# Optimization experiments

Measured on AMD Instinct MI355X. Metric: run time of the kernel, lower is better.

Reference implementation:

```python
import math
import jax, jax.numpy as jnp
import numpy as np

S, B, H = 2048, 1, 4096
NH, HD = 32, 128          # heads, head dim
ROT = HD // 2             # rotary dim per 2D-RoPE half = 64


def rotate_half(x):
    x1, x2 = jnp.split(x, 2, axis=-1)
    return jnp.concatenate([-x2, x1], axis=-1)


def rope_tables(seq_len, dim, base=10000.0):
    inv_freq = 1.0 / (base ** (jnp.arange(0, dim, 2, dtype=jnp.float32) / dim))
    freqs = jnp.arange(seq_len, dtype=jnp.float32)[:, None] * inv_freq[None, :]
    emb = jnp.concatenate([freqs, freqs], axis=-1)  # [S, dim]
    return jnp.cos(emb), jnp.sin(emb)


def apply_rope(q, k, cos, sin, pos):
    # q,k: [S,B,NH,ROT]; pos: [S,B] -> gather cos/sin per token
    c = cos[pos][:, :, None, :]  # [S,B,1,ROT]
    s = sin[pos][:, :, None, :]
    return q * c + rotate_half(q) * s, k * c + rotate_half(k) * s


def setup_inputs() -> dict:
    key = jax.random.key(0)
    ks = jax.random.split(key, 5)
    hidden_states = jax.random.normal(ks[0], (S, B, H), dtype=jnp.float32)
    pos = jnp.arange(S, dtype=jnp.int64 if jax.config.jax_enable_x64 else jnp.int32)
    position_ids = jnp.stack([pos, pos])[None]  # [B=1, 2, S]
    attention_mask = jnp.triu(jnp.ones((S, S), dtype=bool), k=1)[None, None]  # True = masked
    scale = 0.02
    wqkv = jax.random.normal(ks[1], (3 * H, H), dtype=jnp.float32) * scale
    bqkv = jax.random.normal(ks[2], (3 * H,), dtype=jnp.float32) * scale
    wdense = jax.random.normal(ks[3], (H, H), dtype=jnp.float32) * scale
    bdense = jax.random.normal(ks[4], (H,), dtype=jnp.float32) * scale
    return {"hidden_states": hidden_states, "position_ids": position_ids,
            "attention_mask": attention_mask, "wqkv": wqkv, "bqkv": bqkv,
            "wdense": wdense, "bdense": bdense, "layer_id": 1}


def reference(hidden_states, position_ids, attention_mask, wqkv, bqkv, wdense, bdense, layer_id):
    s, b, h = hidden_states.shape
    # fused QKV projection: [S,B,NH,3*HD]
    mixed = (jnp.einsum('sbh,oh->sbo', hidden_states, wqkv) + bqkv).reshape(s, b, NH, 3 * HD)
    q, k, v = jnp.split(mixed, 3, axis=-1)  # each [S,B,NH,HD]

    # 2D RoPE: split head dim in half, rotate each half with its own position ids
    q1, q2 = jnp.split(q, 2, axis=-1)
    k1, k2 = jnp.split(k, 2, axis=-1)
    cos, sin = rope_tables(s, ROT)
    pos = position_ids[:, 0, :].T       # [S,B]
    block_pos = position_ids[:, 1, :].T  # [S,B]
    q1, k1 = apply_rope(q1, k1, cos, sin, pos)
    q2, k2 = apply_rope(q2, k2, cos, sin, block_pos)
    q = jnp.concatenate([q1, q2], axis=-1)
    k = jnp.concatenate([k1, k2], axis=-1)

    # layer-scaled attention (ChatGLM style)
    coeff = float(layer_id + 1)
    q = q / (math.sqrt(HD) * coeff)
    scores = jnp.einsum('sbhd,tbhd->bhst', q, k)  # [B,NH,S,S]
    scores = jnp.where(attention_mask, jnp.float32(-10000.0), scores)
    scores = scores.astype(jnp.float32) * coeff
    probs = jax.nn.softmax(scores, axis=-1).astype(q.dtype)
    context = jnp.einsum('bhst,tbhd->sbhd', probs, v).reshape(s, b, h)

    out = jnp.einsum('sbh,oh->sbo', context, wdense) + bdense
    return out
```

## Files before the change

kernel.cpp:

```cpp
#include <hip/hip_runtime.h>

typedef unsigned short u16;
typedef unsigned int u32;
typedef __attribute__((ext_vector_type(4))) float f32x4;
typedef __attribute__((ext_vector_type(16))) float f32x16;
typedef __attribute__((ext_vector_type(8))) short bf16x8;
typedef __attribute__((ext_vector_type(2))) unsigned int u32x2;

#define S_LEN 2048
#define NHEAD 32
#define HDD 128
#define HID 4096
#define N_QKV 12288
#define KDIM 4096
#define RS 12288

__device__ __forceinline__ u16 f2bf(float f) {
  u32 u = __builtin_bit_cast(u32, f);
  u = (u + 0x7FFFu + ((u >> 16) & 1u)) >> 16;
  return (u16)u;
}
__device__ __forceinline__ float bf2f(u16 h) {
  u32 u = ((u32)h) << 16;
  return __builtin_bit_cast(float, u);
}

__device__ __forceinline__ int gkey(int line) { return (line ^ (line >> 1)) & 7; }

__device__ __forceinline__ void gl2lds16(const void* g, void* l) {
  __builtin_amdgcn_global_load_lds(
      (const __attribute__((address_space(1))) u32*)g,
      (__attribute__((address_space(3))) u32*)l, 16, 0, 0);
}

#define FULL_BAR()                          \
  {                                         \
    asm volatile("" ::: "memory");          \
    __builtin_amdgcn_s_barrier();           \
    asm volatile("" ::: "memory");          \
  }

__global__ __launch_bounds__(256) void cvt3_kernel(const float* __restrict__ s0, u16* __restrict__ d0, int n0,
                                                   const float* __restrict__ s2, u16* __restrict__ d2, int n2,
                                                   float* __restrict__ cos_t, float* __restrict__ sin_t) {
  int i = blockIdx.x * blockDim.x + threadIdx.x;
  if (i < S_LEN * 32) {
    int s = i >> 5, ii = i & 31;
    float invf = expf(-0.28782313662425572f * (float)ii);
    float a = (float)s * invf;
    cos_t[i] = cosf(a);
    sin_t[i] = sinf(a);
  }
  int st = gridDim.x * blockDim.x;
  int ntot = n0 + n2;
  for (; i < ntot; i += st) {
    const float* s;
    u16* d;
    int j = i;
    if (j < n0) {
      s = s0; d = d0;
    } else {
      j -= n0; s = s2; d = d2;
    }
    float4 v = ((const float4*)s)[j];
    u32x2 o;
    o.x = (u32)f2bf(v.x) | ((u32)f2bf(v.y) << 16);
    o.y = (u32)f2bf(v.z) | ((u32)f2bf(v.w) << 16);
    ((u32x2*)d)[j] = o;
  }
}

__global__ __launch_bounds__(256) void ropek_kernel(u16* __restrict__ mixed,
                                                    const int* __restrict__ pid,
                                                    const float* __restrict__ cos_t,
                                                    const float* __restrict__ sin_t) {
  int idx = blockIdx.x * blockDim.x + threadIdx.x;
  const int total = NHEAD * S_LEN * 2 * 8;
  if (idx >= total) return;
  int j = idx & 7;
  int half = (idx >> 3) & 1;
  int s = (idx >> 4) & (S_LEN - 1);
  int h = idx >> 15;
  int i0 = j * 4;
  int p = pid[half * S_LEN + s];
  float4 c4 = *(const float4*)(cos_t + p * 32 + i0);
  float4 s4 = *(const float4*)(sin_t + p * 32 + i0);
  u16* base = mixed + (size_t)s * RS + h * 384 + 128 + half * 64 + i0;
  ushort4 x1v = *(const ushort4*)(base);
  ushort4 x2v = *(const ushort4*)(base + 32);
  ushort4 o1, o2;
  {
    float x1 = bf2f(x1v.x), x2 = bf2f(x2v.x);
    o1.x = f2bf(x1 * c4.x - x2 * s4.x);
    o2.x = f2bf(x2 * c4.x + x1 * s4.x);
  }
  {
    float x1 = bf2f(x1v.y), x2 = bf2f(x2v.y);
    o1.y = f2bf(x1 * c4.y - x2 * s4.y);
    o2.y = f2bf(x2 * c4.y + x1 * s4.y);
  }
  {
    float x1 = bf2f(x1v.z), x2 = bf2f(x2v.z);
    o1.z = f2bf(x1 * c4.z - x2 * s4.z);
    o2.z = f2bf(x2 * c4.z + x1 * s4.z);
  }
  {
    float x1 = bf2f(x1v.w), x2 = bf2f(x2v.w);
    o1.w = f2bf(x1 * c4.w - x2 * s4.w);
    o2.w = f2bf(x2 * c4.w + x1 * s4.w);
  }
  *(ushort4*)(base) = o1;
  *(ushort4*)(base + 32) = o2;
}

__global__ __launch_bounds__(512, 2) void gemmQ(const u16* __restrict__ A,
                                                const u16* __restrict__ B,
                                                const float* __restrict__ bias,
                                                u16* __restrict__ outb) {
  __shared__ __align__(16) char lds[3][40960];

  const int tid = threadIdx.x;
  const int lane = tid & 63, w = tid >> 6;
  const int l31 = lane & 31, hh = lane >> 5;
  const int wm = w >> 2, wn = w & 3;

  int x = blockIdx.x & 7, loc = blockIdx.x >> 3;
  int mb = loc & 7, nb = x * 4 + (loc >> 3);
  const int bm = mb * 256, bn = nb * 384;

  f32x16 acc[4][3];
#pragma unroll
  for (int mi = 0; mi < 4; ++mi)
#pragma unroll
    for (int ni = 0; ni < 3; ++ni)
#pragma unroll
      for (int r = 0; r < 16; ++r) acc[mi][ni][r] = 0.f;

  const size_t K2 = (size_t)KDIM * 2;

  const char* gA[2];
#pragma unroll
  for (int j = 0; j < 2; ++j) {
    int slot = j * 512 + tid;
    int line = slot >> 3;
    int sl = (slot & 7) ^ gkey(line);
    int row = 2 * line + (sl >> 2);
    int colb = (sl & 3) * 16;
    gA[j] = (const char*)A + (size_t)(bm + row) * K2 + colb;
  }
  const char* gB[3];
#pragma unroll
  for (int j = 0; j < 3; ++j) {
    int slot = j * 512 + tid;
    int line = slot >> 3;
    int sl = (slot & 7) ^ gkey(line);
    int row = 2 * line + (sl >> 2);
    int colb = (sl & 3) * 16;
    gB[j] = (const char*)B + (size_t)(bn + row) * K2 + colb;
  }
  const int ldst = w * 1024;

#define QIA(t, bi)                                                  \
  {                                                                 \
    char* Lb = lds[bi];                                             \
    gl2lds16(gA[0] + (size_t)(t) * 64, Lb + ldst);                  \
    gl2lds16(gA[1] + (size_t)(t) * 64, Lb + 8192 + ldst);           \
  }
#define QIB(t, bi)                                                  \
  {                                                                 \
    char* Lb = lds[bi] + 16384;                                     \
    _Pragma("unroll")                                               \
    for (int j = 0; j < 3; ++j)                                     \
      gl2lds16(gB[j] + (size_t)(t) * 64, Lb + j * 8192 + ldst);     \
  }

  int offA[4][2], offB[3][2];
#pragma unroll
  for (int mi = 0; mi < 4; ++mi) {
    int r = wm * 128 + mi * 32 + l31;
    int line = r >> 1;
#pragma unroll
    for (int kk = 0; kk < 2; ++kk) {
      int sl = (((r & 1) << 2) + kk * 2 + hh) ^ gkey(line);
      offA[mi][kk] = line * 128 + sl * 16;
    }
  }
#pragma unroll
  for (int ni = 0; ni < 3; ++ni) {
    int r = wn * 96 + ni * 32 + l31;
    int line = r >> 1;
#pragma unroll
    for (int kk = 0; kk < 2; ++kk) {
      int sl = (((r & 1) << 2) + kk * 2 + hh) ^ gkey(line);
      offB[ni][kk] = 16384 + line * 128 + sl * 16;
    }
  }

  QIA(0, 0); QIB(0, 0);
  QIA(1, 1); QIB(1, 1);
  asm volatile("s_waitcnt vmcnt(5)" ::: "memory");
  FULL_BAR();

  int cur = 0, nx2 = 2;
  for (int kt = 0; kt < 128; ++kt) {
    const char* buf = lds[cur];
    const bool pf = (kt + 2) < 128;
    bf16x8 a[4], b[3];
#pragma unroll
    for (int mi = 0; mi < 4; ++mi) a[mi] = *(const bf16x8*)(buf + offA[mi][0]);
#pragma unroll
    for (int ni = 0; ni < 3; ++ni) b[ni] = *(const bf16x8*)(buf + offB[ni][0]);
    if (pf) QIA(kt + 2, nx2);
    FULL_BAR();
    __builtin_amdgcn_s_setprio(1);
#pragma unroll
    for (int mi = 0; mi < 4; ++mi)
#pragma unroll
      for (int ni = 0; ni < 3; ++ni)
        acc[mi][ni] = __builtin_amdgcn_mfma_f32_32x32x16_bf16(a[mi], b[ni], acc[mi][ni], 0, 0, 0);
    __builtin_amdgcn_s_setprio(0);
#pragma unroll
    for (int mi = 0; mi < 4; ++mi) a[mi] = *(const bf16x8*)(buf + offA[mi][1]);
#pragma unroll
    for (int ni = 0; ni < 3; ++ni) b[ni] = *(const bf16x8*)(buf + offB[ni][1]);
    if (pf) {
      QIB(kt + 2, nx2);
      asm volatile("s_waitcnt vmcnt(5)" ::: "memory");
    } else if (kt == 126) {
      asm volatile("s_waitcnt vmcnt(0)" ::: "memory");
    }
    FULL_BAR();
    __builtin_amdgcn_s_setprio(1);
#pragma unroll
    for (int mi = 0; mi < 4; ++mi)
#pragma unroll
      for (int ni = 0; ni < 3; ++ni)
        acc[mi][ni] = __builtin_amdgcn_mfma_f32_32x32x16_bf16(a[mi], b[ni], acc[mi][ni], 0, 0, 0);
    __builtin_amdgcn_s_setprio(0);
    cur = (cur + 1 == 3) ? 0 : cur + 1;
    nx2 = (nx2 + 1 == 3) ? 0 : nx2 + 1;
  }
#undef QIA
#undef QIB

#pragma unroll
  for (int ni = 0; ni < 3; ++ni) {
    int n = bn + wn * 96 + ni * 32 + l31;
    float bv = bias[n];
#pragma unroll
    for (int mi = 0; mi < 4; ++mi) {
      int m0 = bm + wm * 128 + mi * 32 + 4 * hh;
#pragma unroll
      for (int reg = 0; reg < 16; ++reg) {
        int row = m0 + (reg & 3) + 8 * (reg >> 2);
        outb[(size_t)row * N_QKV + n] = f2bf(acc[mi][ni][reg] + bv);
      }
    }
  }
}

__global__ __launch_bounds__(512, 2) void gemmD(const u16* __restrict__ A,
                                                const float* __restrict__ Bf,
                                                const float* __restrict__ bias,
                                                float* __restrict__ outf) {
  __shared__ __align__(16) char lds[2][49152];

  const int tid = threadIdx.x;
  const int lane = tid & 63, w = tid >> 6;
  const int l31 = lane & 31, hh = lane >> 5;
  const int wm = w >> 1, wn = w & 1;

  int x = blockIdx.x & 7, loc = blockIdx.x >> 3;
  int mb = loc & 7, nb = x * 4 + (loc >> 3);
  const int bm = mb * 256, bn = nb * 128;

  f32x16 acc[2][2];
#pragma unroll
  for (int mi = 0; mi < 2; ++mi)
#pragma unroll
    for (int ni = 0; ni < 2; ++ni)
#pragma unroll
      for (int r = 0; r < 16; ++r) acc[mi][ni][r] = 0.f;

  const size_t K2 = (size_t)KDIM * 2;

  const char* gA[2];
#pragma unroll
  for (int j = 0; j < 2; ++j) {
    int slot = j * 512 + tid;
    int line = slot >> 3;
    int sl = (slot & 7) ^ gkey(line);
    int row = 2 * line + (sl >> 2);
    int colb = (sl & 3) * 16;
    gA[j] = (const char*)A + (size_t)(bm + row) * K2 + colb;
  }
  int bline = tid >> 3;
  int bsl = tid & 7;
  int brow = 2 * bline + (bsl >> 2);
  int bcole = (bsl & 3) * 8;
  const float* gBs = Bf + (size_t)(bn + brow) * KDIM + bcole;
  int bphys = bsl ^ gkey(bline);
  const int bwr = 32768 + bline * 128 + bphys * 16;
  const int ldst = w * 1024;

#define DIA(t, kk)                                                            \
  {                                                                           \
    char* Lb = lds[(t) & 1] + (kk) * 16384;                                   \
    gl2lds16(gA[0] + (size_t)(t) * 128 + (kk) * 64, Lb + ldst);               \
    gl2lds16(gA[1] + (size_t)(t) * 128 + (kk) * 64, Lb + 8192 + ldst);        \
  }
#define DGB(t)                                                                \
  {                                                                           \
    const float* p0 = gBs + (size_t)(t) * 64;                                 \
    b0a = *(const float4*)(p0);                                               \
    b0b = *(const float4*)(p0 + 4);                                           \
    b1a = *(const float4*)(p0 + 32);                                          \
    b1b = *(const float4*)(p0 + 36);                                          \
  }
#define DWB(t)                                                                \
  {                                                                           \
    bf16x8 o0, o1;                                                            \
    o0[0] = (short)f2bf(b0a.x); o0[1] = (short)f2bf(b0a.y);                   \
    o0[2] = (short)f2bf(b0a.z); o0[3] = (short)f2bf(b0a.w);                   \
    o0[4] = (short)f2bf(b0b.x); o0[5] = (short)f2bf(b0b.y);                   \
    o0[6] = (short)f2bf(b0b.z); o0[7] = (short)f2bf(b0b.w);                   \
    o1[0] = (short)f2bf(b1a.x); o1[1] = (short)f2bf(b1a.y);                   \
    o1[2] = (short)f2bf(b1a.z); o1[3] = (short)f2bf(b1a.w);                   \
    o1[4] = (short)f2bf(b1b.x); o1[5] = (short)f2bf(b1b.y);                   \
    o1[6] = (short)f2bf(b1b.z); o1[7] = (short)f2bf(b1b.w);                   \
    char* Lb = lds[(t) & 1];                                                  \
    *(bf16x8*)(Lb + bwr) = o0;                                                \
    *(bf16x8*)(Lb + 8192 + bwr) = o1;                                         \
  }

  int offA[2][2][2], offB[2][2][2];
#pragma unroll
  for (int mi = 0; mi < 2; ++mi) {
    int r = wm * 64 + mi * 32 + l31;
    int line = r >> 1;
#pragma unroll
    for (int kku = 0; kku < 2; ++kku)
#pragma unroll
      for (int st = 0; st < 2; ++st) {
        int sl = (((r & 1) << 2) + st * 2 + hh) ^ gkey(line);
        offA[mi][kku][st] = kku * 16384 + line * 128 + sl * 16;
      }
  }
#pragma unroll
  for (int ni = 0; ni < 2; ++ni) {
    int r = wn * 64 + ni * 32 + l31;
    int line = r >> 1;
#pragma unroll
    for (int kku = 0; kku < 2; ++kku)
#pragma unroll
      for (int st = 0; st < 2; ++st) {
        int sl = (((r & 1) << 2) + st * 2 + hh) ^ gkey(line);
        offB[ni][kku][st] = 32768 + kku * 8192 + line * 128 + sl * 16;
      }
  }

  float4 b0a, b0b, b1a, b1b;
  DGB(0);
  DIA(0, 0);
  DIA(0, 1);
  asm volatile("s_waitcnt vmcnt(4)" ::: "memory");
  DWB(0);
  asm volatile("s_waitcnt vmcnt(0) lgkmcnt(0)" ::: "memory");
  FULL_BAR();

  for (int kt = 0; kt < 64; ++kt) {
    const char* buf = lds[kt & 1];
    const bool pf = (kt + 1) < 64;
    bf16x8 a[2][2], b[2][2];
#pragma unroll
    for (int mi = 0; mi < 2; ++mi)
#pragma unroll
      for (int st = 0; st < 2; ++st) a[mi][st] = *(const bf16x8*)(buf + offA[mi][0][st]);
#pragma unroll
    for (int ni = 0; ni < 2; ++ni)
#pragma unroll
      for (int st = 0; st < 2; ++st) b[ni][st] = *(const bf16x8*)(buf + offB[ni][0][st]);
    if (pf) {
      DIA(kt + 1, 0);
      DGB(kt + 1);
      asm volatile("s_waitcnt vmcnt(6)" ::: "memory");
    } else {
      asm volatile("s_waitcnt vmcnt(0)" ::: "memory");
    }
    FULL_BAR();
    __builtin_amdgcn_s_setprio(1);
#pragma unroll
    for (int st = 0; st < 2; ++st)
#pragma unroll
      for (int mi = 0; mi < 2; ++mi)
#pragma unroll
        for (int ni = 0; ni < 2; ++ni)
          acc[mi][ni] = __builtin_amdgcn_mfma_f32_32x32x16_bf16(a[mi][st], b[ni][st], acc[mi][ni], 0, 0, 0);
    __builtin_amdgcn_s_setprio(0);
#pragma unroll
    for (int mi = 0; mi < 2; ++mi)
#pragma unroll
      for (int st = 0; st < 2; ++st) a[mi][st] = *(const bf16x8*)(buf + offA[mi][1][st]);
#pragma unroll
    for (int ni = 0; ni < 2; ++ni)
#pragma unroll
      for (int st = 0; st < 2; ++st) b[ni][st] = *(const bf16x8*)(buf + offB[ni][1][st]);
    if (pf) {
      DIA(kt + 1, 1);
      asm volatile("s_waitcnt vmcnt(2)" ::: "memory");
      DWB(kt + 1);
      asm volatile("s_waitcnt lgkmcnt(0)" ::: "memory");
    }
    FULL_BAR();
    __builtin_amdgcn_s_setprio(1);
#pragma unroll
    for (int st = 0; st < 2; ++st)
#pragma unroll
      for (int mi = 0; mi < 2; ++mi)
#pragma unroll
        for (int ni = 0; ni < 2; ++ni)
          acc[mi][ni] = __builtin_amdgcn_mfma_f32_32x32x16_bf16(a[mi][st], b[ni][st], acc[mi][ni], 0, 0, 0);
    __builtin_amdgcn_s_setprio(0);
  }
#undef DIA
#undef DGB
#undef DWB

#pragma unroll
  for (int ni = 0; ni < 2; ++ni) {
    int n = bn + wn * 64 + ni * 32 + l31;
    float bv = bias[n];
#pragma unroll
    for (int mi = 0; mi < 2; ++mi) {
      int m0 = bm + wm * 64 + mi * 32 + 4 * hh;
#pragma unroll
      for (int reg = 0; reg < 16; ++reg) {
        int row = m0 + (reg & 3) + 8 * (reg >> 2);
        outf[(size_t)row * HID + n] = acc[mi][ni][reg] + bv;
      }
    }
  }
}

__global__ __launch_bounds__(512) void attn_kernel(const u16* __restrict__ mixed,
                                                   const int* __restrict__ pid,
                                                   const float* __restrict__ cos_t,
                                                   const float* __restrict__ sin_t,
                                                   u16* __restrict__ ctx) {
  __shared__ __align__(16) u16 Ksh[2][64 * 136];
  __shared__ __align__(16) u16 Vsh[2][128 * 64];
  __shared__ __align__(16) u16 Pt[8][16 * 72];

  int tid = threadIdx.x;
  int lane = tid & 63, w = tid >> 6;
  int lane15 = lane & 15, g = lane >> 4;

  int bpg = blockIdx.x & 7;
  int h = blockIdx.x >> 3;

  const u16* qp = mixed + (size_t)h * 384;
  const u16* kp = mixed + (size_t)h * 384 + 128;
  const u16* vp = mixed + (size_t)h * 384 + 256;

  int krow = tid >> 3, kc = (tid & 7) * 16;
  int vk0 = 2 * (tid & 31), vd0 = (tid >> 5) * 8;
  f32x4 z4 = {0.f, 0.f, 0.f, 0.f};
  const float QSC = 0.08838834764831845f;
  const float L2E = 1.4426950408889634f;

  bf16x8 kx0, kx1, vr0, vr1;
#define ALOAD(t)                                                              \
  {                                                                           \
    const u16* kr = kp + (size_t)((t)*64 + krow) * RS + kc;                   \
    kx0 = *(const bf16x8*)kr;                                                 \
    kx1 = *(const bf16x8*)(kr + 8);                                           \
    const u16* vr = vp + (size_t)((t)*64 + vk0) * RS + vd0;                   \
    vr0 = *(const bf16x8*)vr;                                                 \
    vr1 = *(const bf16x8*)(vr + RS);                                          \
  }
#define AWRITE(bb)                                                            \
  {                                                                           \
    *(bf16x8*)(&Ksh[bb][krow * 136 + kc]) = kx0;                              \
    *(bf16x8*)(&Ksh[bb][krow * 136 + kc + 8]) = kx1;                          \
    _Pragma("unroll") for (int jj = 0; jj < 8; ++jj) {                        \
      int d = vd0 + jj;                                                       \
      u32 val = (u32)(u16)vr0[jj] | ((u32)(u16)vr1[jj] << 16);                \
      *(u32*)((char*)Vsh[bb] + d * 128 + (((vk0 >> 3) ^ (d & 7)) << 4) +      \
              (vk0 & 7) * 2) = val;                                           \
    }                                                                         \
  }

  for (int pass = 0; pass < 2; ++pass) {
    int pg = pass ? (15 - bpg) : bpg;
    int qi = 2 * pg + (w >> 2);
    int qrow = qi * 64 + (w & 3) * 16 + lane15;
    int ntiles = 2 * pg + 2;

    bf16x8 qf[4];
    const u16* qptr = qp + (size_t)qrow * RS + g * 8;
#pragma unroll
    for (int d0 = 0; d0 < 4; ++d0) qf[d0] = *(const bf16x8*)(qptr + d0 * 32);
    {
      int p1 = pid[qrow], p2 = pid[S_LEN + qrow];
      float cc[8], ss[8], dd[8], tt[8];
#pragma unroll
      for (int j = 0; j < 8; ++j) {
        cc[j] = cos_t[p1 * 32 + g * 8 + j];
        ss[j] = sin_t[p1 * 32 + g * 8 + j];
        dd[j] = cos_t[p2 * 32 + g * 8 + j];
        tt[j] = sin_t[p2 * 32 + g * 8 + j];
      }
#pragma unroll
      for (int j = 0; j < 8; ++j) {
        float x1 = bf2f((u16)qf[0][j]), x2 = bf2f((u16)qf[1][j]);
        qf[0][j] = (short)f2bf((x1 * cc[j] - x2 * ss[j]) * QSC);
        qf[1][j] = (short)f2bf((x2 * cc[j] + x1 * ss[j]) * QSC);
        float y1 = bf2f((u16)qf[2][j]), y2 = bf2f((u16)qf[3][j]);
        qf[2][j] = (short)f2bf((y1 * dd[j] - y2 * tt[j]) * QSC);
        qf[3][j] = (short)f2bf((y2 * dd[j] + y1 * tt[j]) * QSC);
      }
    }

    f32x4 pv[8];
#pragma unroll
    for (int db = 0; db < 8; ++db) pv[db] = z4;
    float m_run = -1e30f, l_run = 0.0f;

    ALOAD(0);
    AWRITE(0);
    __syncthreads();

    for (int t = 0; t < ntiles; ++t) {
      const u16* Kc = Ksh[t & 1];
      const char* Vc = (const char*)Vsh[t & 1];
      if (t + 1 < ntiles) ALOAD(t + 1);

      int kb0 = t * 64;
      f32x4 sa[4];
#pragma unroll
      for (int kt16 = 0; kt16 < 4; ++kt16) sa[kt16] = z4;
#pragma unroll
      for (int kt16 = 0; kt16 < 4; ++kt16)
#pragma unroll
        for (int d0 = 0; d0 < 4; ++d0) {
          bf16x8 kf = *(const bf16x8*)(Kc + (kt16 * 16 + lane15) * 136 + d0 * 32 + g * 8);
          sa[kt16] = __builtin_amdgcn_mfma_f32_16x16x32_bf16(kf, qf[d0], sa[kt16], 0, 0, 0);
        }
      float s[16];
#pragma unroll
      for (int kt16 = 0; kt16 < 4; ++kt16)
#pragma unroll
        for (int rr = 0; rr < 4; ++rr) {
          int kg = kb0 + kt16 * 16 + 4 * g + rr;
          s[kt16 * 4 + rr] = (kg > qrow) ? -1e30f : sa[kt16][rr];
        }
      float mx = s[0];
#pragma unroll
      for (int i2 = 1; i2 < 16; ++i2) mx = fmaxf(mx, s[i2]);
      mx = fmaxf(mx, __shfl_xor(mx, 16));
      mx = fmaxf(mx, __shfl_xor(mx, 32));
      if (!__all(mx - m_run <= 8.0f)) {
        float mnew = fmaxf(m_run, mx);
        float fac = exp2f((m_run - mnew) * L2E);
        l_run *= fac;
#pragma unroll
        for (int db = 0; db < 8; ++db) pv[db] *= fac;
        m_run = mnew;
      }
      float p[16], psum = 0.f;
#pragma unroll
      for (int i2 = 0; i2 < 16; ++i2) {
        p[i2] = exp2f((s[i2] - m_run) * L2E);
        psum += p[i2];
      }
      psum += __shfl_xor(psum, 16);
      psum += __shfl_xor(psum, 32);
      l_run += psum;

#pragma unroll
      for (int kt16 = 0; kt16 < 4; ++kt16) {
        u32x2 pw;
        pw.x = (u32)f2bf(p[kt16 * 4 + 0]) | ((u32)f2bf(p[kt16 * 4 + 1]) << 16);
        pw.y = (u32)f2bf(p[kt16 * 4 + 2]) | ((u32)f2bf(p[kt16 * 4 + 3]) << 16);
        *(u32x2*)(&Pt[w][lane15 * 72 + kt16 * 16 + 4 * g]) = pw;
      }
      asm volatile("s_waitcnt lgkmcnt(0)" ::: "memory");
      bf16x8 pf0 = *(const bf16x8*)(&Pt[w][lane15 * 72 + 8 * g]);
      bf16x8 pf1 = *(const bf16x8*)(&Pt[w][lane15 * 72 + 32 + 8 * g]);

#pragma unroll
      for (int db = 0; db < 8; ++db) {
        int d = db * 16 + lane15;
        bf16x8 vf0 = *(const bf16x8*)(Vc + d * 128 + ((g ^ (d & 7)) << 4));
        bf16x8 vf1 = *(const bf16x8*)(Vc + d * 128 + (((4 + g) ^ (d & 7)) << 4));
        pv[db] = __builtin_amdgcn_mfma_f32_16x16x32_bf16(vf0, pf0, pv[db], 0, 0, 0);
        pv[db] = __builtin_amdgcn_mfma_f32_16x16x32_bf16(vf1, pf1, pv[db], 0, 0, 0);
      }

      if (t + 1 < ntiles) AWRITE((t + 1) & 1);
      __syncthreads();
    }

    float inv = 1.0f / l_run;
#pragma unroll
    for (int db = 0; db < 8; ++db) {
      ushort4 o;
      o.x = f2bf(pv[db][0] * inv);
      o.y = f2bf(pv[db][1] * inv);
      o.z = f2bf(pv[db][2] * inv);
      o.w = f2bf(pv[db][3] * inv);
      *(ushort4*)(ctx + (size_t)qrow * HID + h * HDD + db * 16 + 4 * g) = o;
    }
    __syncthreads();
  }
#undef ALOAD
#undef AWRITE
}

extern "C" void kernel_launch(void* const* d_in, const int* in_sizes, int n_in,
                              void* d_out, int out_size, void* d_ws, size_t ws_size,
                              hipStream_t stream) {
  const float* hidden = (const float*)d_in[0];
  const int* pid = (const int*)d_in[1];
  const float* wqkv = (const float*)d_in[3];
  const float* bqkv = (const float*)d_in[4];
  const float* wdense = (const float*)d_in[5];
  const float* bdense = (const float*)d_in[6];
  float* out = (float*)d_out;

  char* ws = (char*)d_ws;
  u16* W1 = (u16*)ws;
  u16* X = (u16*)(ws + 134217728);
  u16* mixed = (u16*)(ws + 150994944);
  u16* ctx = (u16*)(ws + 201326592);
  float* cos_t = (float*)(ws + 218103808);
  float* sin_t = (float*)(ws + 218365952);

  cvt3_kernel<<<dim3(2048), dim3(256), 0, stream>>>(
      wqkv, W1, N_QKV * KDIM / 4, hidden, X, S_LEN * HID / 4, cos_t, sin_t);

  gemmQ<<<dim3(256), dim3(512), 0, stream>>>(X, W1, bqkv, mixed);

  ropek_kernel<<<dim3(4096), dim3(256), 0, stream>>>(mixed, pid, cos_t, sin_t);

  attn_kernel<<<dim3(256), dim3(512), 0, stream>>>(mixed, pid, cos_t, sin_t, ctx);

  gemmD<<<dim3(256), dim3(512), 0, stream>>>(ctx, wdense, bdense, out);
}
```

Measured before the change: 453.9 us.

## Split attention into one 64-row query tile per block, heaviest tiles first

Attention work is reorganized from 256 blocks of 512 threads, each running two balanced passes over paired causal query groups, into 1024 blocks of 256 threads. Each block handles a single 64-row query tile, and blocks are ordered so the longest causal tiles launch first. K/V staging is widened so each thread loads more data per tile. The log2(e) factor is also folded into the Q scale, which removes multiplies from the softmax exponent path. The change gives the scheduler more blocks to balance and likely higher occupancy, at the cost of each K/V tile being reloaded by more blocks.

```diff
diff --git a/kernel.cpp b/kernel.cpp
--- a/kernel.cpp
+++ b/kernel.cpp
@@ -442,176 +442,174 @@
   }
 }
 
-__global__ __launch_bounds__(512) void attn_kernel(const u16* __restrict__ mixed,
+__global__ __launch_bounds__(256) void attn_kernel(const u16* __restrict__ mixed,
                                                    const int* __restrict__ pid,
                                                    const float* __restrict__ cos_t,
                                                    const float* __restrict__ sin_t,
                                                    u16* __restrict__ ctx) {
   __shared__ __align__(16) u16 Ksh[2][64 * 136];
   __shared__ __align__(16) u16 Vsh[2][128 * 64];
-  __shared__ __align__(16) u16 Pt[8][16 * 72];
+  __shared__ __align__(16) u16 Pt[4][16 * 72];
 
   int tid = threadIdx.x;
   int lane = tid & 63, w = tid >> 6;
   int lane15 = lane & 15, g = lane >> 4;
 
-  int bpg = blockIdx.x & 7;
-  int h = blockIdx.x >> 3;
+  int qslot = blockIdx.x >> 5;
+  int h = blockIdx.x & 31;
+  int qi = 31 - qslot;
+  int qrow = qi * 64 + w * 16 + lane15;
+  int ntiles = qi + 1;
 
   const u16* qp = mixed + (size_t)h * 384;
   const u16* kp = mixed + (size_t)h * 384 + 128;
   const u16* vp = mixed + (size_t)h * 384 + 256;
 
-  int krow = tid >> 3, kc = (tid & 7) * 16;
-  int vk0 = 2 * (tid & 31), vd0 = (tid >> 5) * 8;
+  int krow = tid >> 2, kc = (tid & 3) * 32;
+  int vk0 = 2 * (tid & 31), vd0 = (tid >> 5) * 16;
   f32x4 z4 = {0.f, 0.f, 0.f, 0.f};
-  const float QSC = 0.08838834764831845f;
-  const float L2E = 1.4426950408889634f;
-
-  bf16x8 kx0, kx1, vr0, vr1;
+  const float QSCL = 0.08838834764831845f * 1.4426950408889634f;
+
+  bf16x8 kx[4], vr0a, vr0b, vr1a, vr1b;
 #define ALOAD(t)                                                              \
   {                                                                           \
-    const u16* kr = kp + (size_t)((t)*64 + krow) * RS + kc;                   \
-    kx0 = *(const bf16x8*)kr;                                                 \
-    kx1 = *(const bf16x8*)(kr + 8);                                           \
-    const u16* vr = vp + (size_t)((t)*64 + vk0) * RS + vd0;                   \
-    vr0 = *(const bf16x8*)vr;                                                 \
-    vr1 = *(const bf16x8*)(vr + RS);                                          \
+    const bf16x8* kr = (const bf16x8*)(kp + (size_t)((t)*64 + krow) * RS + kc); \
+    kx[0] = kr[0]; kx[1] = kr[1]; kx[2] = kr[2]; kx[3] = kr[3];               \
+    const bf16x8* vr = (const bf16x8*)(vp + (size_t)((t)*64 + vk0) * RS + vd0); \
+    vr0a = vr[0]; vr0b = vr[1];                                               \
+    const bf16x8* vs = (const bf16x8*)(vp + (size_t)((t)*64 + vk0 + 1) * RS + vd0); \
+    vr1a = vs[0]; vr1b = vs[1];                                               \
   }
 #define AWRITE(bb)                                                            \
   {                                                                           \
-    *(bf16x8*)(&Ksh[bb][krow * 136 + kc]) = kx0;                              \
-    *(bf16x8*)(&Ksh[bb][krow * 136 + kc + 8]) = kx1;                          \
+    _Pragma("unroll") for (int c = 0; c < 4; ++c)                             \
+        *(bf16x8*)(&Ksh[bb][krow * 136 + kc + c * 8]) = kx[c];                \
     _Pragma("unroll") for (int jj = 0; jj < 8; ++jj) {                        \
       int d = vd0 + jj;                                                       \
-      u32 val = (u32)(u16)vr0[jj] | ((u32)(u16)vr1[jj] << 16);                \
+      u32 v0 = (u32)(u16)vr0a[jj] | ((u32)(u16)vr1a[jj] << 16);               \
       *(u32*)((char*)Vsh[bb] + d * 128 + (((vk0 >> 3) ^ (d & 7)) << 4) +      \
-              (vk0 & 7) * 2) = val;                                           \
+              (vk0 & 7) * 2) = v0;                                            \
+      int d2 = vd0 + 8 + jj;                                                  \
+      u32 v1 = (u32)(u16)vr0b[jj] | ((u32)(u16)vr1b[jj] << 16);               \
+      *(u32*)((char*)Vsh[bb] + d2 * 128 + (((vk0 >> 3) ^ (d2 & 7)) << 4) +    \
+              (vk0 & 7) * 2) = v1;                                            \
     }                                                                         \
   }
 
-  for (int pass = 0; pass < 2; ++pass) {
-    int pg = pass ? (15 - bpg) : bpg;
-    int qi = 2 * pg + (w >> 2);
-    int qrow = qi * 64 + (w & 3) * 16 + lane15;
-    int ntiles = 2 * pg + 2;
-
-    bf16x8 qf[4];
-    const u16* qptr = qp + (size_t)qrow * RS + g * 8;
-#pragma unroll
-    for (int d0 = 0; d0 < 4; ++d0) qf[d0] = *(const bf16x8*)(qptr + d0 * 32);
-    {
-      int p1 = pid[qrow], p2 = pid[S_LEN + qrow];
-      float cc[8], ss[8], dd[8], tt[8];
-#pragma unroll
-      for (int j = 0; j < 8; ++j) {
-        cc[j] = cos_t[p1 * 32 + g * 8 + j];
-        ss[j] = sin_t[p1 * 32 + g * 8 + j];
-        dd[j] = cos_t[p2 * 32 + g * 8 + j];
-        tt[j] = sin_t[p2 * 32 + g * 8 + j];
+  bf16x8 qf[4];
+  const u16* qptr = qp + (size_t)qrow * RS + g * 8;
+#pragma unroll
+  for (int d0 = 0; d0 < 4; ++d0) qf[d0] = *(const bf16x8*)(qptr + d0 * 32);
+  {
+    int p1 = pid[qrow], p2 = pid[S_LEN + qrow];
+    float cc[8], ss[8], dd[8], tt[8];
+#pragma unroll
+    for (int j = 0; j < 8; ++j) {
+      cc[j] = cos_t[p1 * 32 + g * 8 + j];
+      ss[j] = sin_t[p1 * 32 + g * 8 + j];
+      dd[j] = cos_t[p2 * 32 + g * 8 + j];
+      tt[j] = sin_t[p2 * 32 + g * 8 + j];
+    }
+#pragma unroll
+    for (int j = 0; j < 8; ++j) {
+      float x1 = bf2f((u16)qf[0][j]), x2 = bf2f((u16)qf[1][j]);
+      qf[0][j] = (short)f2bf((x1 * cc[j] - x2 * ss[j]) * QSCL);
+      qf[1][j] = (short)f2bf((x2 * cc[j] + x1 * ss[j]) * QSCL);
+      float y1 = bf2f((u16)qf[2][j]), y2 = bf2f((u16)qf[3][j]);
+      qf[2][j] = (short)f2bf((y1 * dd[j] - y2 * tt[j]) * QSCL);
+      qf[3][j] = (short)f2bf((y2 * dd[j] + y1 * tt[j]) * QSCL);
+    }
+  }
+
+  f32x4 pv[8];
+#pragma unroll
+  for (int db = 0; db < 8; ++db) pv[db] = z4;
+  float m_run = -1e30f, l_run = 0.0f;
+
+  ALOAD(0);
+  AWRITE(0);
+  __syncthreads();
+
+  for (int t = 0; t < ntiles; ++t) {
+    const u16* Kc = Ksh[t & 1];
+    const char* Vc = (const char*)Vsh[t & 1];
+    if (t + 1 < ntiles) ALOAD(t + 1);
+
+    int kb0 = t * 64;
+    f32x4 sa[4];
+#pragma unroll
+    for (int kt16 = 0; kt16 < 4; ++kt16) sa[kt16] = z4;
+#pragma unroll
+    for (int kt16 = 0; kt16 < 4; ++kt16)
+#pragma unroll
+      for (int d0 = 0; d0 < 4; ++d0) {
+        bf16x8 kf = *(const bf16x8*)(Kc + (kt16 * 16 + lane15) * 136 + d0 * 32 + g * 8);
+        sa[kt16] = __builtin_amdgcn_mfma_f32_16x16x32_bf16(kf, qf[d0], sa[kt16], 0, 0, 0);
       }
-#pragma unroll
-      for (int j = 0; j < 8; ++j) {
-        float x1 = bf2f((u16)qf[0][j]), x2 = bf2f((u16)qf[1][j]);
-        qf[0][j] = (short)f2bf((x1 * cc[j] - x2 * ss[j]) * QSC);
-        qf[1][j] = (short)f2bf((x2 * cc[j] + x1 * ss[j]) * QSC);
-        float y1 = bf2f((u16)qf[2][j]), y2 = bf2f((u16)qf[3][j]);
-        qf[2][j] = (short)f2bf((y1 * dd[j] - y2 * tt[j]) * QSC);
-        qf[3][j] = (short)f2bf((y2 * dd[j] + y1 * tt[j]) * QSC);
+    float s[16];
+#pragma unroll
+    for (int kt16 = 0; kt16 < 4; ++kt16)
+#pragma unroll
+      for (int rr = 0; rr < 4; ++rr) {
+        int kg = kb0 + kt16 * 16 + 4 * g + rr;
+        s[kt16 * 4 + rr] = (kg > qrow) ? -1e30f : sa[kt16][rr];
       }
-    }
-
-    f32x4 pv[8];
-#pragma unroll
-    for (int db = 0; db < 8; ++db) pv[db] = z4;
-    float m_run = -1e30f, l_run = 0.0f;
-
-    ALOAD(0);
-    AWRITE(0);
+    float mx = s[0];
+#pragma unroll
+    for (int i2 = 1; i2 < 16; ++i2) mx = fmaxf(mx, s[i2]);
+    mx = fmaxf(mx, __shfl_xor(mx, 16));
+    mx = fmaxf(mx, __shfl_xor(mx, 32));
+    if (!__all(mx - m_run <= 8.0f)) {
+      float mnew = fmaxf(m_run, mx);
+      float fac = exp2f(m_run - mnew);
+      l_run *= fac;
+#pragma unroll
+      for (int db = 0; db < 8; ++db) pv[db] *= fac;
+      m_run = mnew;
+    }
+    float p[16], psum = 0.f;
+#pragma unroll
+    for (int i2 = 0; i2 < 16; ++i2) {
+      p[i2] = exp2f(s[i2] - m_run);
+      psum += p[i2];
+    }
+    psum += __shfl_xor(psum, 16);
+    psum += __shfl_xor(psum, 32);
+    l_run += psum;
+
+#pragma unroll
+    for (int kt16 = 0; kt16 < 4; ++kt16) {
+      u32x2 pw;
+      pw.x = (u32)f2bf(p[kt16 * 4 + 0]) | ((u32)f2bf(p[kt16 * 4 + 1]) << 16);
+      pw.y = (u32)f2bf(p[kt16 * 4 + 2]) | ((u32)f2bf(p[kt16 * 4 + 3]) << 16);
+      *(u32x2*)(&Pt[w][lane15 * 72 + kt16 * 16 + 4 * g]) = pw;
+    }
+    asm volatile("s_waitcnt lgkmcnt(0)" ::: "memory");
+    bf16x8 pf0 = *(const bf16x8*)(&Pt[w][lane15 * 72 + 8 * g]);
+    bf16x8 pf1 = *(const bf16x8*)(&Pt[w][lane15 * 72 + 32 + 8 * g]);
+
+#pragma unroll
+    for (int db = 0; db < 8; ++db) {
+      int d = db * 16 + lane15;
+      bf16x8 vf0 = *(const bf16x8*)(Vc + d * 128 + ((g ^ (d & 7)) << 4));
+      bf16x8 vf1 = *(const bf16x8*)(Vc + d * 128 + (((4 + g) ^ (d & 7)) << 4));
+      pv[db] = __builtin_amdgcn_mfma_f32_16x16x32_bf16(vf0, pf0, pv[db], 0, 0, 0);
+      pv[db] = __builtin_amdgcn_mfma_f32_16x16x32_bf16(vf1, pf1, pv[db], 0, 0, 0);
+    }
+
+    if (t + 1 < ntiles) AWRITE((t + 1) & 1);
     __syncthreads();
-
-    for (int t = 0; t < ntiles; ++t) {
-      const u16* Kc = Ksh[t & 1];
-      const char* Vc = (const char*)Vsh[t & 1];
-      if (t + 1 < ntiles) ALOAD(t + 1);
-
-      int kb0 = t * 64;
-      f32x4 sa[4];
-#pragma unroll
-      for (int kt16 = 0; kt16 < 4; ++kt16) sa[kt16] = z4;
-#pragma unroll
-      for (int kt16 = 0; kt16 < 4; ++kt16)
-#pragma unroll
-        for (int d0 = 0; d0 < 4; ++d0) {
-          bf16x8 kf = *(const bf16x8*)(Kc + (kt16 * 16 + lane15) * 136 + d0 * 32 + g * 8);
-          sa[kt16] = __builtin_amdgcn_mfma_f32_16x16x32_bf16(kf, qf[d0], sa[kt16], 0, 0, 0);
-        }
-      float s[16];
-#pragma unroll
-      for (int kt16 = 0; kt16 < 4; ++kt16)
-#pragma unroll
-        for (int rr = 0; rr < 4; ++rr) {
-          int kg = kb0 + kt16 * 16 + 4 * g + rr;
-          s[kt16 * 4 + rr] = (kg > qrow) ? -1e30f : sa[kt16][rr];
-        }
-      float mx = s[0];
-#pragma unroll
-      for (int i2 = 1; i2 < 16; ++i2) mx = fmaxf(mx, s[i2]);
-      mx = fmaxf(mx, __shfl_xor(mx, 16));
-      mx = fmaxf(mx, __shfl_xor(mx, 32));
-      if (!__all(mx - m_run <= 8.0f)) {
-        float mnew = fmaxf(m_run, mx);
-        float fac = exp2f((m_run - mnew) * L2E);
-        l_run *= fac;
-#pragma unroll
-        for (int db = 0; db < 8; ++db) pv[db] *= fac;
-        m_run = mnew;
-      }
-      float p[16], psum = 0.f;
-#pragma unroll
-      for (int i2 = 0; i2 < 16; ++i2) {
-        p[i2] = exp2f((s[i2] - m_run) * L2E);
-        psum += p[i2];
-      }
-      psum += __shfl_xor(psum, 16);
-      psum += __shfl_xor(psum, 32);
-      l_run += psum;
-
-#pragma unroll
-      for (int kt16 = 0; kt16 < 4; ++kt16) {
-        u32x2 pw;
-        pw.x = (u32)f2bf(p[kt16 * 4 + 0]) | ((u32)f2bf(p[kt16 * 4 + 1]) << 16);
-        pw.y = (u32)f2bf(p[kt16 * 4 + 2]) | ((u32)f2bf(p[kt16 * 4 + 3]) << 16);
-        *(u32x2*)(&Pt[w][lane15 * 72 + kt16 * 16 + 4 * g]) = pw;
-      }
-      asm volatile("s_waitcnt lgkmcnt(0)" ::: "memory");
-      bf16x8 pf0 = *(const bf16x8*)(&Pt[w][lane15 * 72 + 8 * g]);
-      bf16x8 pf1 = *(const bf16x8*)(&Pt[w][lane15 * 72 + 32 + 8 * g]);
-
-#pragma unroll
-      for (int db = 0; db < 8; ++db) {
-        int d = db * 16 + lane15;
-        bf16x8 vf0 = *(const bf16x8*)(Vc + d * 128 + ((g ^ (d & 7)) << 4));
-        bf16x8 vf1 = *(const bf16x8*)(Vc + d * 128 + (((4 + g) ^ (d & 7)) << 4));
-        pv[db] = __builtin_amdgcn_mfma_f32_16x16x32_bf16(vf0, pf0, pv[db], 0, 0, 0);
-        pv[db] = __builtin_amdgcn_mfma_f32_16x16x32_bf16(vf1, pf1, pv[db], 0, 0, 0);
-      }
-
-      if (t + 1 < ntiles) AWRITE((t + 1) & 1);
-      __syncthreads();
-    }
-
-    float inv = 1.0f / l_run;
-#pragma unroll
-    for (int db = 0; db < 8; ++db) {
-      ushort4 o;
-      o.x = f2bf(pv[db][0] * inv);
-      o.y = f2bf(pv[db][1] * inv);
-      o.z = f2bf(pv[db][2] * inv);
-      o.w = f2bf(pv[db][3] * inv);
-      *(ushort4*)(ctx + (size_t)qrow * HID + h * HDD + db * 16 + 4 * g) = o;
-    }
-    __syncthreads();
+  }
+
+  float inv = 1.0f / l_run;
+#pragma unroll
+  for (int db = 0; db < 8; ++db) {
+    ushort4 o;
+    o.x = f2bf(pv[db][0] * inv);
+    o.y = f2bf(pv[db][1] * inv);
+    o.z = f2bf(pv[db][2] * inv);
+    o.w = f2bf(pv[db][3] * inv);
+    *(ushort4*)(ctx + (size_t)qrow * HID + h * HDD + db * 16 + 4 * g) = o;
   }
 #undef ALOAD
 #undef AWRITE
@@ -643,7 +641,7 @@
 
   ropek_kernel<<<dim3(4096), dim3(256), 0, stream>>>(mixed, pid, cos_t, sin_t);
 
-  attn_kernel<<<dim3(256), dim3(512), 0, stream>>>(mixed, pid, cos_t, sin_t, ctx);
+  attn_kernel<<<dim3(1024), dim3(256), 0, stream>>>(mixed, pid, cos_t, sin_t, ctx);
 
   gemmD<<<dim3(256), dim3(512), 0, stream>>>(ctx, wdense, bdense, out);
 }
```

After: 467.0 us. 2.9% more time.
